# Optimization experiments

Measured on AMD Instinct MI355X. Metric: run time of the kernel, lower is better.

## Reference

```python
import jax, jax.numpy as jnp
import numpy as np

HIDDEN_DIM = 64
MEMORY_SLOTS = 8
SEQ_LEN = 64
VOCAB_SIZE = 64
B = 524288


def setup_inputs() -> dict:
    key = jax.random.key(0)
    k1, k2, k3, k4, k5, k6 = jax.random.split(key, 6)
    seqs = jax.random.randint(k1, (B, SEQ_LEN), 0, VOCAB_SIZE + 2, dtype=jnp.int64 if jax.config.jax_enable_x64 else jnp.int32)
    query_tok = jax.random.randint(k2, (B,), 0, VOCAB_SIZE + 2, dtype=seqs.dtype)
    embed = jax.random.normal(k3, (VOCAB_SIZE + 2, HIDDEN_DIM), dtype=jnp.float32)
    # torch Linear: y = x @ W.T + b
    W1 = jax.random.normal(k4, (HIDDEN_DIM, HIDDEN_DIM * 2), dtype=jnp.float32) * (1.0 / np.sqrt(HIDDEN_DIM * 2))
    b1 = jnp.zeros((HIDDEN_DIM,), dtype=jnp.float32)
    W2 = jax.random.normal(k5, (VOCAB_SIZE, HIDDEN_DIM), dtype=jnp.float32) * (1.0 / np.sqrt(HIDDEN_DIM))
    b2 = jnp.zeros((VOCAB_SIZE,), dtype=jnp.float32)
    return {"seqs": seqs, "query_tok": query_tok, "embed": embed,
            "W1": W1, "b1": b1, "W2": W2, "b2": b2}


def reference(seqs, query_tok, embed, W1, b1, W2, b2):
    # FIFO of capacity MEMORY_SLOTS over tokens t=0..SEQ_LEN-2 keeps exactly the
    # last MEMORY_SLOTS tokens: positions [SEQ_LEN-1-MEMORY_SLOTS, SEQ_LEN-1).
    win = seqs[:, SEQ_LEN - 1 - MEMORY_SLOTS : SEQ_LEN - 1]        # [B, 8]
    mem_summary = embed[win].mean(axis=1)                          # [B, H]
    q_emb = embed[query_tok]                                       # [B, H]
    h = jnp.concatenate([q_emb, mem_summary], axis=-1)             # [B, 2H]
    h = jax.nn.relu(h @ W1.T + b1)                                 # [B, H]
    logits = h @ W2.T + b2                                         # [B, VOCAB]
    return logits
```

## Files before the change

### kernel.cpp

```cpp
#include <hip/hip_runtime.h>

#define HID 64
#define NTOK 66
#define SEQ 64
#define WIN0 55
#define NW 8
#define LDS_STRIDE 72
#define ITERS 8
#define ROWS_PER_ITER 64

typedef _Float16 half8 __attribute__((ext_vector_type(8)));
typedef unsigned short ushort8v __attribute__((ext_vector_type(8)));
typedef float float4v __attribute__((ext_vector_type(4)));

static __device__ __forceinline__ unsigned short f2h(float f) {
    _Float16 h = (_Float16)f;
    union { _Float16 h; unsigned short u; } v; v.h = h;
    return v.u;
}

__global__ void build_tables(const float* __restrict__ embed,
                             const float* __restrict__ W1,
                             const float* __restrict__ b1,
                             unsigned short* __restrict__ tbl) {
    int b = blockIdx.x;
    int tb = b & 1;
    int t  = b >> 1;
    int n  = threadIdx.x;
    float acc = tb ? 0.0f : b1[n];
    const float* er = embed + t * HID;
    const float* wr = W1 + n * (2 * HID) + tb * HID;
#pragma unroll 8
    for (int k = 0; k < HID; ++k) acc += er[k] * wr[k];
    if (tb) acc *= 0.125f;
    tbl[tb * (NTOK * HID) + t * HID + n] = f2h(acc);
}

static __device__ __forceinline__ half8 build_hfrag(
    const unsigned short* T_lds, int q, const int* w, int k0c) {
    half8 acc = *(const half8*)(T_lds + q * LDS_STRIDE + k0c);
#pragma unroll
    for (int j = 0; j < NW; ++j)
        acc += *(const half8*)(T_lds + NTOK * LDS_STRIDE + w[j] * LDS_STRIDE + k0c);
    half8 z = (half8)(_Float16)0;
    return __builtin_elementwise_max(acc, z);
}

__global__ __launch_bounds__(256, 4) void fused_forward(
    const int* __restrict__ seqs,
    const int* __restrict__ qtok,
    const float* __restrict__ W2,
    const float* __restrict__ b2,
    const unsigned short* __restrict__ tbl,
    float* __restrict__ out)
{
    __shared__ unsigned short T_lds[2 * NTOK * LDS_STRIDE];

    int tid  = threadIdx.x;
    int wv   = tid >> 6;
    int l    = tid & 63;
    int lrow = l & 15;
    int lg   = l >> 4;
    int lk8  = lg * 8;

    int row0 = blockIdx.x * (ITERS * ROWS_PER_ITER) + wv * 16 + lrow;

#define LOADT(s, t_) { \
    int row_ = row0 + (t_) * ROWS_PER_ITER; \
    q##s = qtok[row_]; \
    const int* sp_ = seqs + row_ * SEQ + WIN0; \
    _Pragma("unroll") \
    for (int j = 0; j < NW; ++j) w##s[j] = sp_[j]; \
}

#define COMPUTE(s, t_) { \
    half8 a0 = build_hfrag(T_lds, q##s, w##s, lk8); \
    half8 a1 = build_hfrag(T_lds, q##s, w##s, 32 + lk8); \
    float* op = out + (size_t)(row0 + (t_) * ROWS_PER_ITER) * HID; \
    _Pragma("unroll") \
    for (int nt = 0; nt < 4; ++nt) { \
        float4v acc = b2v[nt]; \
        acc = __builtin_amdgcn_mfma_f32_16x16x32_f16(wfrag[nt][0], a0, acc, 0, 0, 0); \
        acc = __builtin_amdgcn_mfma_f32_16x16x32_f16(wfrag[nt][1], a1, acc, 0, 0, 0); \
        *(float4v*)(op + nt * 16 + lg * 4) = acc; \
    } \
}

    int qA, qB;
    int wA[NW], wB[NW];

    LOADT(A, 0);
    LOADT(B, 1);

    half8   wfrag[4][2];
    float4v b2v[4];
#pragma unroll
    for (int nt = 0; nt < 4; ++nt) {
        b2v[nt] = *(const float4v*)(b2 + nt * 16 + lg * 4);
#pragma unroll
        for (int kc = 0; kc < 2; ++kc) {
            const float* wp = W2 + (nt * 16 + lrow) * HID + kc * 32 + lk8;
            half8 f;
#pragma unroll
            for (int j = 0; j < 8; ++j) f[j] = (_Float16)wp[j];
            wfrag[nt][kc] = f;
        }
    }

    for (int i = tid; i < 2 * NTOK * (HID / 8); i += 256) {
        int tbi = i / (NTOK * 8);
        int rem = i - tbi * (NTOK * 8);
        int t   = rem >> 3;
        int kq  = (rem & 7) << 3;
        *(ushort8v*)(T_lds + tbi * (NTOK * LDS_STRIDE) + t * LDS_STRIDE + kq) =
            *(const ushort8v*)(tbl + tbi * (NTOK * HID) + t * HID + kq);
    }
    __syncthreads();

    COMPUTE(A, 0); LOADT(A, 2);
    COMPUTE(B, 1); LOADT(B, 3);
    COMPUTE(A, 2); LOADT(A, 4);
    COMPUTE(B, 3); LOADT(B, 5);
    COMPUTE(A, 4); LOADT(A, 6);
    COMPUTE(B, 5); LOADT(B, 7);
    COMPUTE(A, 6);
    COMPUTE(B, 7);

#undef LOADT
#undef COMPUTE
}

extern "C" void kernel_launch(void* const* d_in, const int* in_sizes, int n_in,
                              void* d_out, int out_size, void* d_ws, size_t ws_size,
                              hipStream_t stream) {
    const int*   seqs  = (const int*)d_in[0];
    const int*   qtok  = (const int*)d_in[1];
    const float* embed = (const float*)d_in[2];
    const float* W1    = (const float*)d_in[3];
    const float* b1    = (const float*)d_in[4];
    const float* W2    = (const float*)d_in[5];
    const float* b2    = (const float*)d_in[6];
    float* out = (float*)d_out;
    unsigned short* tbl = (unsigned short*)d_ws;

    int B = in_sizes[0] / SEQ;

    build_tables<<<NTOK * 2, HID, 0, stream>>>(embed, W1, b1, tbl);

    int grid = B / (ITERS * ROWS_PER_ITER);
    fused_forward<<<grid, 256, 0, stream>>>(seqs, qtok, W2, b2, tbl, out);
}
```

Measured before the change: 50.49 us.

## Software-pipeline LDS gathers one half-fragment ahead of the MFMA work

Restructures the per-iteration compute so the nine LDS row gathers for the next half-fragment (the next K-half of the same row group, or the first half of the following row group) are issued while the current half is summed and fed to MFMAs. Splits the MFMA chain into K0 and K1 phases with the gathers for the next step in between. The aim is to hide LDS latency behind the ALU adds and MFMA work. The cost is more live registers (nine half8 buffers plus accumulators), which could hurt occupancy under launch_bounds(256,4).

```diff
diff --git a/kernel.cpp b/kernel.cpp
--- a/kernel.cpp
+++ b/kernel.cpp
@@ -36,16 +36,6 @@
     tbl[tb * (NTOK * HID) + t * HID + n] = f2h(acc);
 }
 
-static __device__ __forceinline__ half8 build_hfrag(
-    const unsigned short* T_lds, int q, const int* w, int k0c) {
-    half8 acc = *(const half8*)(T_lds + q * LDS_STRIDE + k0c);
-#pragma unroll
-    for (int j = 0; j < NW; ++j)
-        acc += *(const half8*)(T_lds + NTOK * LDS_STRIDE + w[j] * LDS_STRIDE + k0c);
-    half8 z = (half8)(_Float16)0;
-    return __builtin_elementwise_max(acc, z);
-}
-
 __global__ __launch_bounds__(256, 4) void fused_forward(
     const int* __restrict__ seqs,
     const int* __restrict__ qtok,
@@ -65,6 +55,12 @@
 
     int row0 = blockIdx.x * (ITERS * ROWS_PER_ITER) + wv * 16 + lrow;
 
+    int qA, qB;
+    int wA[NW], wB[NW];
+    half8  g[9];
+    half8  a0, a1;
+    float4v acc4[4];
+
 #define LOADT(s, t_) { \
     int row_ = row0 + (t_) * ROWS_PER_ITER; \
     q##s = qtok[row_]; \
@@ -73,21 +69,67 @@
     for (int j = 0; j < NW; ++j) w##s[j] = sp_[j]; \
 }
 
-#define COMPUTE(s, t_) { \
-    half8 a0 = build_hfrag(T_lds, q##s, w##s, lk8); \
-    half8 a1 = build_hfrag(T_lds, q##s, w##s, 32 + lk8); \
+#define GATHER_ALL(qq, ww, k0c) { \
+    g[8] = *(const half8*)(T_lds + (qq) * LDS_STRIDE + (k0c)); \
+    _Pragma("unroll") \
+    for (int j = 0; j < NW; ++j) \
+        g[j] = *(const half8*)(T_lds + NTOK * LDS_STRIDE + (ww)[j] * LDS_STRIDE + (k0c)); \
+}
+
+#define SUM_REISSUE(aout, qq, ww, k0c) { \
+    half8 s_ = g[8]; \
+    g[8] = *(const half8*)(T_lds + (qq) * LDS_STRIDE + (k0c)); \
+    _Pragma("unroll") \
+    for (int j = 0; j < NW; ++j) { \
+        s_ += g[j]; \
+        g[j] = *(const half8*)(T_lds + NTOK * LDS_STRIDE + (ww)[j] * LDS_STRIDE + (k0c)); \
+    } \
+    half8 z_ = (half8)(_Float16)0; \
+    aout = __builtin_elementwise_max(s_, z_); \
+}
+
+#define SUM_FINAL(aout) { \
+    half8 s_ = g[8]; \
+    _Pragma("unroll") \
+    for (int j = 0; j < NW; ++j) s_ += g[j]; \
+    half8 z_ = (half8)(_Float16)0; \
+    aout = __builtin_elementwise_max(s_, z_); \
+}
+
+#define MFMA_K0 { \
+    _Pragma("unroll") \
+    for (int nt = 0; nt < 4; ++nt) \
+        acc4[nt] = __builtin_amdgcn_mfma_f32_16x16x32_f16(wfrag[nt][0], a0, b2v[nt], 0, 0, 0); \
+}
+
+#define MFMA_K1_ST(t_) { \
     float* op = out + (size_t)(row0 + (t_) * ROWS_PER_ITER) * HID; \
     _Pragma("unroll") \
     for (int nt = 0; nt < 4; ++nt) { \
-        float4v acc = b2v[nt]; \
-        acc = __builtin_amdgcn_mfma_f32_16x16x32_f16(wfrag[nt][0], a0, acc, 0, 0, 0); \
-        acc = __builtin_amdgcn_mfma_f32_16x16x32_f16(wfrag[nt][1], a1, acc, 0, 0, 0); \
-        *(float4v*)(op + nt * 16 + lg * 4) = acc; \
+        acc4[nt] = __builtin_amdgcn_mfma_f32_16x16x32_f16(wfrag[nt][1], a1, acc4[nt], 0, 0, 0); \
+        *(float4v*)(op + nt * 16 + lg * 4) = acc4[nt]; \
     } \
 }
 
-    int qA, qB;
-    int wA[NW], wB[NW];
+#define ITER_MID(C, N, t_) { \
+    SUM_REISSUE(a0, q##C, w##C, 32 + lk8); \
+    MFMA_K0; \
+    SUM_REISSUE(a1, q##N, w##N, lk8); \
+    MFMA_K1_ST(t_); \
+    LOADT(C, (t_) + 2); \
+}
+#define ITER_NOLOAD(C, N, t_) { \
+    SUM_REISSUE(a0, q##C, w##C, 32 + lk8); \
+    MFMA_K0; \
+    SUM_REISSUE(a1, q##N, w##N, lk8); \
+    MFMA_K1_ST(t_); \
+}
+#define ITER_LAST(C, t_) { \
+    SUM_REISSUE(a0, q##C, w##C, 32 + lk8); \
+    MFMA_K0; \
+    SUM_FINAL(a1); \
+    MFMA_K1_ST(t_); \
+}
 
     LOADT(A, 0);
     LOADT(B, 1);
@@ -117,17 +159,26 @@
     }
     __syncthreads();
 
-    COMPUTE(A, 0); LOADT(A, 2);
-    COMPUTE(B, 1); LOADT(B, 3);
-    COMPUTE(A, 2); LOADT(A, 4);
-    COMPUTE(B, 3); LOADT(B, 5);
-    COMPUTE(A, 4); LOADT(A, 6);
-    COMPUTE(B, 5); LOADT(B, 7);
-    COMPUTE(A, 6);
-    COMPUTE(B, 7);
+    GATHER_ALL(qA, wA, lk8);
+
+    ITER_MID(A, B, 0);
+    ITER_MID(B, A, 1);
+    ITER_MID(A, B, 2);
+    ITER_MID(B, A, 3);
+    ITER_MID(A, B, 4);
+    ITER_MID(B, A, 5);
+    ITER_NOLOAD(A, B, 6);
+    ITER_LAST(B, 7);
 
 #undef LOADT
-#undef COMPUTE
+#undef GATHER_ALL
+#undef SUM_REISSUE
+#undef SUM_FINAL
+#undef MFMA_K0
+#undef MFMA_K1_ST
+#undef ITER_MID
+#undef ITER_NOLOAD
+#undef ITER_LAST
 }
 
 extern "C" void kernel_launch(void* const* d_in, const int* in_sizes, int n_in,
```

Result: slower. 85.12 us (+68.6%).
